# Kernel optimization log

Hardware: AMD Instinct MI355X
Metric: run time of the kernel (lower is better)

The kernel has to match this reference:

```python
import jax, jax.numpy as jnp
import numpy as np

B, C, H, W = 32, 320, 64, 64
CTX_DIM, CTX_HW = 1024, 16


def _conv3x3(x, w, b):
    # x: [b, cin, h, w], w: [cout, cin, 3, 3] (OIHW), stride 1, SAME padding
    y = jax.lax.conv_general_dilated(x, w, window_strides=(1, 1), padding='SAME',
                                     dimension_numbers=('NCHW', 'OIHW', 'NCHW'))
    return y + b[None, :, None, None]


def setup_inputs() -> dict:
    key = jax.random.key(0)
    ks = jax.random.split(key, 8)
    global_x = jax.random.normal(ks[0], (B, C, H, W), jnp.float32)
    context = jax.random.normal(ks[1], (B, CTX_HW * CTX_HW, CTX_DIM), jnp.float32)
    indicator = jax.random.randint(ks[2], (B, 2), 0, 2).astype(jnp.float32)
    # bbox = (x1, y1, x2, y2) normalized; keep boxes inside [0,1) so no sample
    # hits the torch try/except skip path, but sizes vary per sample.
    lo = jax.random.uniform(ks[3], (B, 2), minval=0.0, maxval=0.4)
    ext = jax.random.uniform(ks[4], (B, 2), minval=0.1, maxval=0.55)
    bbox = jnp.concatenate([lo, lo + ext], axis=1)
    # params (local_proj_out is zero-init in the source; we use small random
    # weights so the baseline is non-degenerate)
    w_in = jax.random.normal(ks[5], (C, CTX_DIM + 2, 3, 3), jnp.float32) * 0.02
    b_in = jnp.zeros((C,), jnp.float32)
    w_out = jax.random.normal(ks[6], (C, C, 3, 3), jnp.float32) * 0.02
    b_out = jnp.zeros((C,), jnp.float32)
    return {'global_x': global_x, 'context': context, 'indicator': indicator,
            'bbox': bbox, 'w_in': w_in, 'b_in': b_in, 'w_out': w_out, 'b_out': b_out}


def reference(global_x, context, indicator, bbox, w_in, b_in, w_out, b_out):
    b, c, h, w = global_x.shape
    # 'b (h w) c -> b c h w' with h=16
    ctx = context.reshape(b, CTX_HW, CTX_HW, -1).transpose(0, 3, 1, 2)
    ind_map = jnp.broadcast_to(indicator[:, :, None, None], (b, 2, CTX_HW, CTX_HW))
    ctx = jnp.concatenate([ctx, ind_map], axis=1)  # [b, ctx_dim+2, 16, 16]
    cx = _conv3x3(ctx, w_in, b_in)
    cx = cx * jax.nn.sigmoid(cx)                    # silu
    cx = _conv3x3(cx, w_out, b_out)                 # [b, c, 16, 16]
    # per-sample ROI nearest-resize + add, fully vectorized (torch loop body)
    bb = (bbox * h).astype(jnp.int32)               # truncation like .int()
    x1, y1 = bb[:, 0], bb[:, 1]
    x2 = jnp.maximum(bb[:, 2], x1 + 1)
    y2 = jnp.maximum(bb[:, 3], y1 + 1)
    # torch try/except skips samples where slice shapes mismatch (box off-grid)
    ok = (y2 <= h) & (x2 <= w) & (y1 >= 0) & (x1 >= 0)
    ys = jnp.arange(h)[None, :]
    xs = jnp.arange(w)[None, :]
    # nearest interpolation: src = floor(dst * in_size / out_size)
    src_y = jnp.clip(((ys - y1[:, None]) * CTX_HW) // (y2 - y1)[:, None], 0, CTX_HW - 1)
    src_x = jnp.clip(((xs - x1[:, None]) * CTX_HW) // (x2 - x1)[:, None], 0, CTX_HW - 1)
    vy = (ys >= y1[:, None]) & (ys < y2[:, None])   # [b, h]
    vx = (xs >= x1[:, None]) & (xs < x2[:, None])   # [b, w]
    bi = jnp.arange(b)[:, None, None]
    # gather per output pixel -> [b, h, w, c] -> [b, c, h, w]
    local = cx[bi, :, src_y[:, :, None], src_x[:, None, :]].transpose(0, 3, 1, 2)
    mask = (ok[:, None, None] & vy[:, :, None] & vx[:, None, :])[:, None]  # [b,1,h,w]
    return global_x + jnp.where(mask, local, jnp.zeros((), global_x.dtype))
```

## Files before the change

### kernel.cpp

```cpp
#include <hip/hip_runtime.h>
#include <cstddef>

#define BB 32
#define CC 320
#define HH 64
#define WW 64
#define CTX_HW 16
#define NPIX 256

typedef __attribute__((ext_vector_type(8))) short bf16x8;
typedef __attribute__((ext_vector_type(4))) float f32x4;

__device__ inline ushort f2bf(float x) {
  union { float f; unsigned u; } v; v.f = x;
  unsigned r = v.u + 0x7fff + ((v.u >> 16) & 1);
  return (ushort)(r >> 16);
}

__global__ __launch_bounds__(256) void cast_ctx(
    const float* __restrict__ ctx, const float* __restrict__ ind,
    ushort* __restrict__ ctxP, ushort* __restrict__ cx1P) {
  int b = blockIdx.x, p = blockIdx.y, t = threadIdx.x;
  ushort* orow = ctxP + ((size_t)b * 257 + p) * 1056;
  if (p < 256) {
    const float* irow = ctx + ((size_t)b * 256 + p) * 1024;
    float4 v = ((const float4*)irow)[t];
    ushort4 o;
    o.x = f2bf(v.x); o.y = f2bf(v.y); o.z = f2bf(v.z); o.w = f2bf(v.w);
    ((ushort4*)orow)[t] = o;
    if (t < 32) {
      float val = (t == 0) ? ind[b * 2] : (t == 1) ? ind[b * 2 + 1] : 0.0f;
      orow[1024 + t] = f2bf(val);
    }
  } else {
    ushort4 z = make_ushort4(0, 0, 0, 0);
    for (int i = t; i < 264; i += 256) ((ushort4*)orow)[i] = z;
    if (t < 80) ((ushort4*)(cx1P + ((size_t)b * 257 + 256) * 320))[t] = z;
  }
}

template <int KIN, int KP>
__global__ __launch_bounds__(256) void wt_tr(
    const float* __restrict__ w, ushort* __restrict__ wT) {
  size_t idx = (size_t)blockIdx.x * 256 + threadIdx.x;
  constexpr size_t total = (size_t)9 * 320 * KP;
  if (idx >= total) return;
  int ci = (int)(idx % KP);
  size_t rem = idx / KP;
  int co = (int)(rem % 320);
  int t = (int)(rem / 320);
  float v = (ci < KIN) ? w[((size_t)co * KIN + ci) * 9 + t] : 0.0f;
  wT[idx] = f2bf(v);
}

__global__ __launch_bounds__(64) void prep_maps(
    const float* __restrict__ bbox, int* __restrict__ sy, int* __restrict__ sx) {
  int b = blockIdx.x;
  int t = threadIdx.x;
  int x1 = (int)(bbox[b * 4 + 0] * (float)HH);
  int y1 = (int)(bbox[b * 4 + 1] * (float)HH);
  int x2 = max((int)(bbox[b * 4 + 2] * (float)HH), x1 + 1);
  int y2 = max((int)(bbox[b * 4 + 3] * (float)HH), y1 + 1);
  bool ok = (y2 <= HH) && (x2 <= WW) && (y1 >= 0) && (x1 >= 0);
  int vy = -1, vx = -1;
  if (ok && t >= y1 && t < y2) vy = min(15, max(0, ((t - y1) * CTX_HW) / (y2 - y1)));
  if (ok && t >= x1 && t < x2) vx = min(15, max(0, ((t - x1) * CTX_HW) / (x2 - x1)));
  sy[b * 64 + t] = vy;
  sx[b * 64 + t] = vx;
}

template <int KP, int NCHUNK, int SILU, int PLANAR_OUT>
__global__ __launch_bounds__(512) void conv_mfma(
    const ushort* __restrict__ src, const ushort* __restrict__ wT,
    const float* __restrict__ bias, void* __restrict__ dstv) {
  constexpr int PL = 40;
  __shared__ ushort plane[257 * PL];

  int b = blockIdx.x;
  int co0 = blockIdx.y * 32;
  int tid = threadIdx.x;
  int wid = tid >> 6;
  int lane = tid & 63;
  int m = lane & 15;
  int quad = lane >> 4;
  int mg = wid >> 1;
  int ng = wid & 1;
  int y0 = mg * 4;
  int co = co0 + ng * 16 + m;

  if (tid < PL) plane[256 * PL + tid] = 0;

  f32x4 acc[4];
#pragma unroll
  for (int i = 0; i < 4; ++i) acc[i] = (f32x4)(0.0f);

  const ushort* srcb = src + (size_t)b * 257 * KP;
  int row = tid >> 1, half = tid & 1;
  const ushort* gsrc = srcb + (size_t)row * KP + half * 16;
  ushort* lds_dst = plane + row * PL + half * 16;

  for (int cic = 0; cic < NCHUNK; ++cic) {
    __syncthreads();
    {
      const float4* g = (const float4*)(gsrc + cic * 32);
      float4 v0 = g[0];
      float4 v1 = g[1];
      ((float4*)lds_dst)[0] = v0;
      ((float4*)lds_dst)[1] = v1;
    }
    __syncthreads();
    const ushort* wbase = wT + (size_t)co * KP + cic * 32 + quad * 8;
#pragma unroll
    for (int dx = 0; dx < 3; ++dx) {
      int sx = m + dx - 1;
      bool vx = (unsigned)sx < 16u;
      bf16x8 af[6];
#pragma unroll
      for (int j = 0; j < 6; ++j) {
        int syr = y0 - 1 + j;
        bool v = vx && ((unsigned)syr < 16u);
        int ldsrow = v ? (syr * 16 + sx) : 256;
        af[j] = *(const bf16x8*)(plane + ldsrow * PL + quad * 8);
      }
#pragma unroll
      for (int dy = 0; dy < 3; ++dy) {
        int tap = dy * 3 + dx;
        bf16x8 bf = *(const bf16x8*)(wbase + (size_t)tap * 320 * KP);
#pragma unroll
        for (int mt = 0; mt < 4; ++mt) {
          acc[mt] = __builtin_amdgcn_mfma_f32_16x16x32_bf16(af[mt + dy], bf,
                                                            acc[mt], 0, 0, 0);
        }
      }
    }
  }

  float bv = bias[co];
  if (PLANAR_OUT) {
    float* dst = (float*)dstv;
#pragma unroll
    for (int mt = 0; mt < 4; ++mt) {
      f32x4 v = acc[mt] + bv;
      *(f32x4*)(dst + ((size_t)b * CC + co) * NPIX + (y0 + mt) * 16 + quad * 4) = v;
    }
  } else {
    ushort* dst = (ushort*)dstv;
#pragma unroll
    for (int mt = 0; mt < 4; ++mt) {
#pragma unroll
      for (int r = 0; r < 4; ++r) {
        float v = acc[mt][r] + bv;
        if (SILU) v = v / (1.0f + __expf(-v));
        int p = (y0 + mt) * 16 + quad * 4 + r;
        dst[((size_t)b * 257 + p) * 320 + co] = f2bf(v);
      }
    }
  }
}

__global__ __launch_bounds__(256) void scatter_add(
    const float* __restrict__ gx, const float* __restrict__ cx2,
    const int* __restrict__ sy, const int* __restrict__ sx,
    float* __restrict__ out) {
  int blk = blockIdx.x;
  int part = blk & 3;
  int bc = blk >> 2;
  int b = bc / CC;
  int t = threadIdx.x;
  int e = part * 1024 + t * 4;
  int y = e >> 6, x0 = e & 63;
  size_t idx = (size_t)bc * 4096 + e;
  float4 g = *(const float4*)(gx + idx);
  int vy = sy[b * 64 + y];
  if (vy >= 0) {
    const float* cxp = cx2 + (size_t)bc * NPIX + vy * 16;
    int v0 = sx[b * 64 + x0 + 0]; if (v0 >= 0) g.x += cxp[v0];
    int v1 = sx[b * 64 + x0 + 1]; if (v1 >= 0) g.y += cxp[v1];
    int v2 = sx[b * 64 + x0 + 2]; if (v2 >= 0) g.z += cxp[v2];
    int v3 = sx[b * 64 + x0 + 3]; if (v3 >= 0) g.w += cxp[v3];
  }
  *(float4*)(out + idx) = g;
}

extern "C" void kernel_launch(void* const* d_in, const int* in_sizes, int n_in,
                              void* d_out, int out_size, void* d_ws, size_t ws_size,
                              hipStream_t stream) {
  const float* gx    = (const float*)d_in[0];
  const float* ctx   = (const float*)d_in[1];
  const float* ind   = (const float*)d_in[2];
  const float* bbox  = (const float*)d_in[3];
  const float* w_in  = (const float*)d_in[4];
  const float* b_in  = (const float*)d_in[5];
  const float* w_out = (const float*)d_in[6];
  const float* b_out = (const float*)d_in[7];
  float* out = (float*)d_out;

  char* ws = (char*)d_ws;
  float* cx2   = (float*)ws;  ws += (size_t)BB * CC * NPIX * 4;
  ushort* ctxP = (ushort*)ws; ws += (size_t)BB * 257 * 1056 * 2;
  ushort* wT1  = (ushort*)ws; ws += (size_t)9 * 320 * 1056 * 2;
  ushort* wT2  = (ushort*)ws; ws += (size_t)9 * 320 * 320 * 2;
  ushort* cx1P = (ushort*)ws; ws += (size_t)BB * 257 * 320 * 2;
  int* sy = (int*)ws;         ws += BB * 64 * 4;
  int* sx = (int*)ws;

  cast_ctx<<<dim3(BB, 257), 256, 0, stream>>>(ctx, ind, ctxP, cx1P);
  wt_tr<1026, 1056><<<11880, 256, 0, stream>>>(w_in, wT1);
  wt_tr<320, 320><<<3600, 256, 0, stream>>>(w_out, wT2);
  prep_maps<<<BB, 64, 0, stream>>>(bbox, sy, sx);
  conv_mfma<1056, 33, 1, 0><<<dim3(BB, 10), 512, 0, stream>>>(ctxP, wT1, b_in, (void*)cx1P);
  conv_mfma<320, 10, 0, 1><<<dim3(BB, 10), 512, 0, stream>>>(cx1P, wT2, b_out, (void*)cx2);
  scatter_add<<<BB * CC * 4, 256, 0, stream>>>(gx, cx2, sy, sx, out);
}
```

Measured before the change: 502.8 us.

## Split-K conv with 64-wide channel tiles, separate combine, and per-row weight transpose

Both convolutions now split the input-channel reduction across blockIdx.z (4-way for conv1, 2-way for conv2) and widen each block to 64 output channels, with each wave holding two B fragments. fp32 partial sums go to a workspace. A combine kernel then adds bias, applies SiLU and transposes the result into bf16 pixel-major layout. The scatter kernel sums conv2's two partials and the bias directly. Weight transposition now stages one output channel per block in LDS so global reads are coalesced. The aim is more blocks in flight (the old grid had only 320 blocks) and more reuse of A fragments. The cost is extra fp32 partial traffic and one more launch.

```diff
diff --git a/kernel.cpp b/kernel.cpp
--- a/kernel.cpp
+++ b/kernel.cpp
@@ -42,15 +42,17 @@
 template <int KIN, int KP>
 __global__ __launch_bounds__(256) void wt_tr(
     const float* __restrict__ w, ushort* __restrict__ wT) {
-  size_t idx = (size_t)blockIdx.x * 256 + threadIdx.x;
-  constexpr size_t total = (size_t)9 * 320 * KP;
-  if (idx >= total) return;
-  int ci = (int)(idx % KP);
-  size_t rem = idx / KP;
-  int co = (int)(rem % 320);
-  int t = (int)(rem / 320);
-  float v = (ci < KIN) ? w[((size_t)co * KIN + ci) * 9 + t] : 0.0f;
-  wT[idx] = f2bf(v);
+  __shared__ float wl[KIN * 9];
+  int co = blockIdx.x, t = threadIdx.x;
+  const float* wsrc = w + (size_t)co * KIN * 9;
+  for (int i = t; i < KIN * 9; i += 256) wl[i] = wsrc[i];
+  __syncthreads();
+#pragma unroll
+  for (int tap = 0; tap < 9; ++tap) {
+    ushort* dst = wT + ((size_t)tap * 320 + co) * KP;
+    for (int ci = t; ci < KP; ci += 256)
+      dst[ci] = f2bf(ci < KIN ? wl[ci * 9 + tap] : 0.0f);
+  }
 }
 
 __global__ __launch_bounds__(64) void prep_maps(
@@ -69,37 +71,39 @@
   sx[b * 64 + t] = vx;
 }
 
-template <int KP, int NCHUNK, int SILU, int PLANAR_OUT>
-__global__ __launch_bounds__(512) void conv_mfma(
+template <int KP, int NCH, int KS>
+__global__ __launch_bounds__(512, 4) void conv_part(
     const ushort* __restrict__ src, const ushort* __restrict__ wT,
-    const float* __restrict__ bias, void* __restrict__ dstv) {
+    float* __restrict__ part) {
   constexpr int PL = 40;
   __shared__ ushort plane[257 * PL];
 
   int b = blockIdx.x;
-  int co0 = blockIdx.y * 32;
+  int co0 = blockIdx.y * 64;
+  int z = blockIdx.z;
+  int c0 = z * NCH / KS, c1 = (z + 1) * NCH / KS;
   int tid = threadIdx.x;
-  int wid = tid >> 6;
-  int lane = tid & 63;
-  int m = lane & 15;
-  int quad = lane >> 4;
-  int mg = wid >> 1;
-  int ng = wid & 1;
+  int wid = tid >> 6, lane = tid & 63;
+  int m = lane & 15, quad = lane >> 4;
+  int mg = wid >> 1, ng = wid & 1;
   int y0 = mg * 4;
-  int co = co0 + ng * 16 + m;
+  int coA = co0 + ng * 32 + m;
 
   if (tid < PL) plane[256 * PL + tid] = 0;
 
-  f32x4 acc[4];
-#pragma unroll
-  for (int i = 0; i < 4; ++i) acc[i] = (f32x4)(0.0f);
+  f32x4 acc[4][2];
+#pragma unroll
+  for (int i = 0; i < 4; ++i) {
+    acc[i][0] = (f32x4)(0.0f);
+    acc[i][1] = (f32x4)(0.0f);
+  }
 
   const ushort* srcb = src + (size_t)b * 257 * KP;
   int row = tid >> 1, half = tid & 1;
   const ushort* gsrc = srcb + (size_t)row * KP + half * 16;
   ushort* lds_dst = plane + row * PL + half * 16;
 
-  for (int cic = 0; cic < NCHUNK; ++cic) {
+  for (int cic = c0; cic < c1; ++cic) {
     __syncthreads();
     {
       const float4* g = (const float4*)(gsrc + cic * 32);
@@ -109,63 +113,85 @@
       ((float4*)lds_dst)[1] = v1;
     }
     __syncthreads();
-    const ushort* wbase = wT + (size_t)co * KP + cic * 32 + quad * 8;
+    const ushort* wb0 = wT + (size_t)coA * KP + cic * 32 + quad * 8;
+    const ushort* wb1 = wb0 + (size_t)16 * KP;
 #pragma unroll
     for (int dx = 0; dx < 3; ++dx) {
-      int sx = m + dx - 1;
-      bool vx = (unsigned)sx < 16u;
+      int sxp = m + dx - 1;
+      bool vx = (unsigned)sxp < 16u;
       bf16x8 af[6];
 #pragma unroll
       for (int j = 0; j < 6; ++j) {
         int syr = y0 - 1 + j;
         bool v = vx && ((unsigned)syr < 16u);
-        int ldsrow = v ? (syr * 16 + sx) : 256;
+        int ldsrow = v ? (syr * 16 + sxp) : 256;
         af[j] = *(const bf16x8*)(plane + ldsrow * PL + quad * 8);
       }
 #pragma unroll
       for (int dy = 0; dy < 3; ++dy) {
         int tap = dy * 3 + dx;
-        bf16x8 bf = *(const bf16x8*)(wbase + (size_t)tap * 320 * KP);
+        bf16x8 bf0 = *(const bf16x8*)(wb0 + (size_t)tap * 320 * KP);
+        bf16x8 bf1 = *(const bf16x8*)(wb1 + (size_t)tap * 320 * KP);
 #pragma unroll
         for (int mt = 0; mt < 4; ++mt) {
-          acc[mt] = __builtin_amdgcn_mfma_f32_16x16x32_bf16(af[mt + dy], bf,
-                                                            acc[mt], 0, 0, 0);
+          acc[mt][0] = __builtin_amdgcn_mfma_f32_16x16x32_bf16(af[mt + dy], bf0,
+                                                               acc[mt][0], 0, 0, 0);
+          acc[mt][1] = __builtin_amdgcn_mfma_f32_16x16x32_bf16(af[mt + dy], bf1,
+                                                               acc[mt][1], 0, 0, 0);
         }
       }
     }
   }
 
-  float bv = bias[co];
-  if (PLANAR_OUT) {
-    float* dst = (float*)dstv;
+  float* pz = part + (size_t)z * BB * CC * NPIX + (size_t)b * CC * NPIX;
+#pragma unroll
+  for (int nt = 0; nt < 2; ++nt) {
+    int co = coA + nt * 16;
 #pragma unroll
     for (int mt = 0; mt < 4; ++mt) {
-      f32x4 v = acc[mt] + bv;
-      *(f32x4*)(dst + ((size_t)b * CC + co) * NPIX + (y0 + mt) * 16 + quad * 4) = v;
-    }
-  } else {
-    ushort* dst = (ushort*)dstv;
-#pragma unroll
-    for (int mt = 0; mt < 4; ++mt) {
-#pragma unroll
-      for (int r = 0; r < 4; ++r) {
-        float v = acc[mt][r] + bv;
-        if (SILU) v = v / (1.0f + __expf(-v));
-        int p = (y0 + mt) * 16 + quad * 4 + r;
-        dst[((size_t)b * 257 + p) * 320 + co] = f2bf(v);
-      }
-    }
-  }
+      *(f32x4*)(pz + (size_t)co * NPIX + (y0 + mt) * 16 + quad * 4) = acc[mt][nt];
+    }
+  }
+}
+
+__global__ __launch_bounds__(256) void combine1(
+    const float* __restrict__ part, const float* __restrict__ bias,
+    ushort* __restrict__ cx1P) {
+  __shared__ float tile[64][65];
+  int b = blockIdx.x, co0 = blockIdx.y * 64, px0 = blockIdx.z * 64;
+  int t = threadIdx.x;
+  int tx = t & 63, ty = t >> 6;
+  const float* pb = part + ((size_t)b * CC + co0) * NPIX + px0 + tx;
+  constexpr size_t KSTR = (size_t)BB * CC * NPIX;
+#pragma unroll
+  for (int i = 0; i < 16; ++i) {
+    int cs = ty * 16 + i;
+    const float* p = pb + (size_t)cs * NPIX;
+    float s = p[0] + p[KSTR] + p[2 * KSTR] + p[3 * KSTR] + bias[co0 + cs];
+    s = s / (1.0f + __expf(-s));
+    tile[cs][tx] = s;
+  }
+  __syncthreads();
+  int px = t >> 2, g = t & 3;
+  ushort* dst = cx1P + ((size_t)b * 257 + px0 + px) * 320 + co0 + g * 16;
+  ushort4 o[4];
+#pragma unroll
+  for (int i = 0; i < 16; ++i)
+    ((ushort*)o)[i] = f2bf(tile[g * 16 + i][px]);
+#pragma unroll
+  for (int i = 0; i < 4; ++i) ((ushort4*)dst)[i] = o[i];
 }
 
 __global__ __launch_bounds__(256) void scatter_add(
-    const float* __restrict__ gx, const float* __restrict__ cx2,
+    const float* __restrict__ gx, const float* __restrict__ p0,
+    const float* __restrict__ p1, const float* __restrict__ b_out,
     const int* __restrict__ sy, const int* __restrict__ sx,
     float* __restrict__ out) {
   int blk = blockIdx.x;
   int part = blk & 3;
   int bc = blk >> 2;
   int b = bc / CC;
+  float bo = b_out[bc % CC];
   int t = threadIdx.x;
   int e = part * 1024 + t * 4;
   int y = e >> 6, x0 = e & 63;
@@ -173,11 +199,11 @@
   float4 g = *(const float4*)(gx + idx);
   int vy = sy[b * 64 + y];
   if (vy >= 0) {
-    const float* cxp = cx2 + (size_t)bc * NPIX + vy * 16;
-    int v0 = sx[b * 64 + x0 + 0]; if (v0 >= 0) g.x += cxp[v0];
-    int v1 = sx[b * 64 + x0 + 1]; if (v1 >= 0) g.y += cxp[v1];
-    int v2 = sx[b * 64 + x0 + 2]; if (v2 >= 0) g.z += cxp[v2];
-    int v3 = sx[b * 64 + x0 + 3]; if (v3 >= 0) g.w += cxp[v3];
+    size_t base = (size_t)bc * NPIX + vy * 16;
+    int v0 = sx[b * 64 + x0 + 0]; if (v0 >= 0) g.x += p0[base + v0] + p1[base + v0] + bo;
+    int v1 = sx[b * 64 + x0 + 1]; if (v1 >= 0) g.y += p0[base + v1] + p1[base + v1] + bo;
+    int v2 = sx[b * 64 + x0 + 2]; if (v2 >= 0) g.z += p0[base + v2] + p1[base + v2] + bo;
+    int v3 = sx[b * 64 + x0 + 3]; if (v3 >= 0) g.w += p0[base + v3] + p1[base + v3] + bo;
   }
   *(float4*)(out + idx) = g;
 }
@@ -196,7 +222,9 @@
   float* out = (float*)d_out;
 
   char* ws = (char*)d_ws;
-  float* cx2   = (float*)ws;  ws += (size_t)BB * CC * NPIX * 4;
+  float* part1 = (float*)ws;
+  float* part2 = (float*)ws;
+  ws += (size_t)4 * BB * CC * NPIX * 4;
   ushort* ctxP = (ushort*)ws; ws += (size_t)BB * 257 * 1056 * 2;
   ushort* wT1  = (ushort*)ws; ws += (size_t)9 * 320 * 1056 * 2;
   ushort* wT2  = (ushort*)ws; ws += (size_t)9 * 320 * 320 * 2;
@@ -205,10 +233,12 @@
   int* sx = (int*)ws;
 
   cast_ctx<<<dim3(BB, 257), 256, 0, stream>>>(ctx, ind, ctxP, cx1P);
-  wt_tr<1026, 1056><<<11880, 256, 0, stream>>>(w_in, wT1);
-  wt_tr<320, 320><<<3600, 256, 0, stream>>>(w_out, wT2);
+  wt_tr<1026, 1056><<<320, 256, 0, stream>>>(w_in, wT1);
+  wt_tr<320, 320><<<320, 256, 0, stream>>>(w_out, wT2);
   prep_maps<<<BB, 64, 0, stream>>>(bbox, sy, sx);
-  conv_mfma<1056, 33, 1, 0><<<dim3(BB, 10), 512, 0, stream>>>(ctxP, wT1, b_in, (void*)cx1P);
-  conv_mfma<320, 10, 0, 1><<<dim3(BB, 10), 512, 0, stream>>>(cx1P, wT2, b_out, (void*)cx2);
-  scatter_add<<<BB * CC * 4, 256, 0, stream>>>(gx, cx2, sy, sx, out);
-}
+  conv_part<1056, 33, 4><<<dim3(BB, 5, 4), 512, 0, stream>>>(ctxP, wT1, part1);
+  combine1<<<dim3(BB, 5, 4), 256, 0, stream>>>(part1, b_in, cx1P);
+  conv_part<320, 10, 2><<<dim3(BB, 5, 2), 512, 0, stream>>>(cx1P, wT2, part2);
+  scatter_add<<<BB * CC * 4, 256, 0, stream>>>(gx, part2, part2 + (size_t)BB * CC * NPIX,
+                                               b_out, sy, sx, out);
+}
```

Measured after the change: 509.7 us. Within noise of the previous version (+1.4%).
